# Performance work log

Hardware: AMD Instinct MI355X
Metric: run time of the kernel (lower is better)

## Reference

```python
import jax, jax.numpy as jnp
import numpy as np
from jax import lax

I, H, C = 1086, 16, 15


def _lstm_layer(x, w_ih, w_hh, b):
    # x: [B, T, in], w_ih: [4H, in], w_hh: [4H, H], b: [4H]  (b = b_ih + b_hh)
    B = x.shape[0]
    Hd = w_hh.shape[1]
    # precompute the big input projection outside the scan
    pre = jnp.einsum('bti,gi->btg', x, w_ih) + b  # [B, T, 4H]

    def step(carry, pt):
        h, c = carry
        gates = pt + h @ w_hh.T  # [B, 4H]
        i, f, g, o = jnp.split(gates, 4, axis=-1)  # torch gate order i,f,g,o
        i = jax.nn.sigmoid(i)
        f = jax.nn.sigmoid(f)
        g = jnp.tanh(g)
        o = jax.nn.sigmoid(o)
        c = f * c + i * g
        h = o * jnp.tanh(c)
        return (h, c), h

    h0 = jnp.zeros((B, Hd), x.dtype)
    c0 = jnp.zeros((B, Hd), x.dtype)
    _, ys = lax.scan(step, (h0, c0), jnp.swapaxes(pre, 0, 1))
    return jnp.swapaxes(ys, 0, 1)  # [B, T, H]


def setup_inputs() -> dict:
    key = jax.random.key(0)
    ks = jax.random.split(key, 20)
    s = 1.0 / np.sqrt(H)  # torch LSTM/Linear default init scale
    x = jax.random.normal(ks[0], (256, 200, I), dtype=jnp.float32)

    def w(k, shape):
        return jax.random.uniform(k, shape, jnp.float32, -s, s)

    inp = {'x': x}
    ins = [I, H, H, H]  # lstm1 layer0/1, lstm2 layer0/1
    names = ['l0a', 'l0b', 'l1a', 'l1b']
    ki = 1
    for n, d_in in zip(names, ins):
        inp['w_ih_' + n] = w(ks[ki], (4 * H, d_in)); ki += 1
        inp['w_hh_' + n] = w(ks[ki], (4 * H, H)); ki += 1
        inp['b_' + n] = w(ks[ki], (4 * H,)); ki += 1
    inp['w_fc1'] = w(ks[ki], (H, H)); ki += 1
    inp['b_fc1'] = w(ks[ki], (H,)); ki += 1
    inp['w_fc2'] = w(ks[ki], (C, H)); ki += 1
    inp['b_fc2'] = w(ks[ki], (C,))
    return inp


def reference(x, w_ih_l0a, w_hh_l0a, b_l0a, w_ih_l0b, w_hh_l0b, b_l0b,
              w_ih_l1a, w_hh_l1a, b_l1a, w_ih_l1b, w_hh_l1b, b_l1b,
              w_fc1, b_fc1, w_fc2, b_fc2):
    # lstm1 (2 layers), dropout between layers is identity in eval mode
    out = _lstm_layer(x, w_ih_l0a, w_hh_l0a, b_l0a)
    out = _lstm_layer(out, w_ih_l0b, w_hh_l0b, b_l0b)
    # lstm2 (2 layers)
    out = _lstm_layer(out, w_ih_l1a, w_hh_l1a, b_l1a)
    out = _lstm_layer(out, w_ih_l1b, w_hh_l1b, b_l1b)
    h_last = out[:, -1, :]  # [B, H]
    h = jax.nn.relu(h_last @ w_fc1.T + b_fc1)
    logits = h @ w_fc2.T + b_fc2  # [B, C]
    return jax.nn.softmax(logits, axis=1)
```

## Files before the change

### kernel.cpp

```cpp
#include <hip/hip_runtime.h>

#define T_STEPS 200
#define IN_DIM 1086

using f32x4v = __attribute__((ext_vector_type(4))) float;
using bf16x8 = __attribute__((ext_vector_type(8))) short;
using u32x4  = __attribute__((ext_vector_type(4))) unsigned int;
typedef unsigned uv2 __attribute__((ext_vector_type(2)));

#if __has_builtin(__builtin_amdgcn_permlane16_swap) && __has_builtin(__builtin_amdgcn_permlane32_swap)
#define HAVE_PERMLANE_SWAP 1
#else
#define HAVE_PERMLANE_SWAP 0
#endif

#if __has_builtin(__builtin_amdgcn_exp2f)
#define EXP2F(x) __builtin_amdgcn_exp2f(x)
#else
#define EXP2F(x) exp2f(x)
#endif

__device__ __forceinline__ float rl_f(float v, int lane) {
    return __uint_as_float((unsigned)__builtin_amdgcn_readlane((int)__float_as_uint(v), lane));
}

__global__ __launch_bounds__(256) void pre0_gemm(
    const float* __restrict__ X, const float* __restrict__ W,
    const float* __restrict__ bias, float* __restrict__ out)
{
    __shared__ unsigned short AhL[4][128][8];
    __shared__ unsigned short AlL[4][128][8];
    __shared__ unsigned short BhL[4][64][8];
    __shared__ unsigned short BlL[4][64][8];

    const int tid  = threadIdx.x;
    const int lane = tid & 63;
    const int wv   = tid >> 6;
    const long m0  = (long)blockIdx.x * 128;

    const int sr  = tid >> 1;
    const int skb = (tid & 1) * 16;
    const int wr  = sr & 63;
    const float* xsrc = X + (m0 + sr) * (long)IN_DIM + skb;
    const float* wsrc = W + (long)wr * IN_DIM + skb;

    const int fr = lane & 15;
    const int kg = lane >> 4;

    f32x4v acc[2][4];
    #pragma unroll
    for (int mf = 0; mf < 2; ++mf)
        #pragma unroll
        for (int nf = 0; nf < 4; ++nf)
            #pragma unroll
            for (int r = 0; r < 4; ++r) acc[mf][nf][r] = 0.0f;

    for (int k0 = 0; k0 < IN_DIM; k0 += 32) {
        float xv[16];
        #pragma unroll
        for (int j = 0; j < 16; j += 2) {
            int k = k0 + skb + j;
            if (k + 2 <= IN_DIM) {
                float2 t = *(const float2*)(xsrc + k0 + j);
                xv[j] = t.x; xv[j + 1] = t.y;
            } else { xv[j] = 0.0f; xv[j + 1] = 0.0f; }
        }
        float wvv[16];
        if (tid < 128) {
            #pragma unroll
            for (int j = 0; j < 16; j += 2) {
                int k = k0 + skb + j;
                if (k + 2 <= IN_DIM) {
                    float2 t = *(const float2*)(wsrc + k0 + j);
                    wvv[j] = t.x; wvv[j + 1] = t.y;
                } else { wvv[j] = 0.0f; wvv[j + 1] = 0.0f; }
            }
        }
        __syncthreads();

        #pragma unroll
        for (int q = 0; q < 2; ++q) {
            u32x4 hw, lw;
            #pragma unroll
            for (int p = 0; p < 4; ++p) {
                float a0 = xv[q * 8 + 2 * p], a1 = xv[q * 8 + 2 * p + 1];
                unsigned u0 = __float_as_uint(a0), u1 = __float_as_uint(a1);
                unsigned h0 = u0 & 0xffff0000u, h1 = u1 & 0xffff0000u;
                hw[p] = (u0 >> 16) | h1;
                float l0 = a0 - __uint_as_float(h0);
                float l1 = a1 - __uint_as_float(h1);
                lw[p] = (__float_as_uint(l0) >> 16) | (__float_as_uint(l1) & 0xffff0000u);
            }
            int kgs = (tid & 1) * 2 + q;
            *(u32x4*)&AhL[kgs][sr][0] = hw;
            *(u32x4*)&AlL[kgs][sr][0] = lw;
        }
        if (tid < 128) {
            #pragma unroll
            for (int q = 0; q < 2; ++q) {
                u32x4 hw, lw;
                #pragma unroll
                for (int p = 0; p < 4; ++p) {
                    float a0 = wvv[q * 8 + 2 * p], a1 = wvv[q * 8 + 2 * p + 1];
                    unsigned u0 = __float_as_uint(a0), u1 = __float_as_uint(a1);
                    unsigned h0 = u0 & 0xffff0000u, h1 = u1 & 0xffff0000u;
                    hw[p] = (u0 >> 16) | h1;
                    float l0 = a0 - __uint_as_float(h0);
                    float l1 = a1 - __uint_as_float(h1);
                    lw[p] = (__float_as_uint(l0) >> 16) | (__float_as_uint(l1) & 0xffff0000u);
                }
                int kgs = (tid & 1) * 2 + q;
                *(u32x4*)&BhL[kgs][wr][0] = hw;
                *(u32x4*)&BlL[kgs][wr][0] = lw;
            }
        }
        __syncthreads();

        bf16x8 ah[2], al[2], bh[4], bl[4];
        #pragma unroll
        for (int mf = 0; mf < 2; ++mf) {
            ah[mf] = *(const bf16x8*)&AhL[kg][wv * 32 + mf * 16 + fr][0];
            al[mf] = *(const bf16x8*)&AlL[kg][wv * 32 + mf * 16 + fr][0];
        }
        #pragma unroll
        for (int nf = 0; nf < 4; ++nf) {
            bh[nf] = *(const bf16x8*)&BhL[kg][nf * 16 + fr][0];
            bl[nf] = *(const bf16x8*)&BlL[kg][nf * 16 + fr][0];
        }
        #pragma unroll
        for (int mf = 0; mf < 2; ++mf)
            #pragma unroll
            for (int nf = 0; nf < 4; ++nf) {
                acc[mf][nf] = __builtin_amdgcn_mfma_f32_16x16x32_bf16(ah[mf], bh[nf], acc[mf][nf], 0, 0, 0);
                acc[mf][nf] = __builtin_amdgcn_mfma_f32_16x16x32_bf16(al[mf], bh[nf], acc[mf][nf], 0, 0, 0);
                acc[mf][nf] = __builtin_amdgcn_mfma_f32_16x16x32_bf16(ah[mf], bl[nf], acc[mf][nf], 0, 0, 0);
            }
    }

    float bvv[4];
    #pragma unroll
    for (int nf = 0; nf < 4; ++nf) bvv[nf] = bias[nf * 16 + fr];
    #pragma unroll
    for (int mf = 0; mf < 2; ++mf)
        #pragma unroll
        for (int nf = 0; nf < 4; ++nf)
            #pragma unroll
            for (int r = 0; r < 4; ++r) {
                long row = m0 + wv * 32 + mf * 16 + kg * 4 + r;
                out[row * 64 + nf * 16 + fr] = acc[mf][nf][r] + bvv[nf];
            }
}

__global__ __launch_bounds__(256) void mega_scan(
    const float* __restrict__ pre0, const float* __restrict__ whh0,
    const float* __restrict__ wih1, const float* __restrict__ whh1, const float* __restrict__ b1,
    const float* __restrict__ wih2, const float* __restrict__ whh2, const float* __restrict__ b2,
    const float* __restrict__ wih3, const float* __restrict__ whh3, const float* __restrict__ b3,
    const float* __restrict__ w_fc1, const float* __restrict__ b_fc1,
    const float* __restrict__ w_fc2, const float* __restrict__ b_fc2,
    float* __restrict__ out)
{
    __shared__ float buf[3][T_STEPS][16];

    const int b    = blockIdx.x;
    const int tid  = threadIdx.x;
    const int g    = tid & 63;
    const int wv   = tid >> 6;

    bool sel16 = false, sel32 = false;
#if HAVE_PERMLANE_SWAP
    {
        uv2 q16 = __builtin_amdgcn_permlane16_swap((unsigned)g, (unsigned)g, false, false);
        sel16 = (__builtin_amdgcn_readfirstlane((int)q16[1]) == 16);
        uv2 q32 = __builtin_amdgcn_permlane32_swap((unsigned)g, (unsigned)g, false, false);
        sel32 = (__builtin_amdgcn_readfirstlane((int)q32[1]) == 32);
    }
#endif

    const float* wih = nullptr; const float* whh; const float* bias = nullptr;
    if      (wv == 0) { whh = whh0; }
    else if (wv == 1) { wih = wih1; whh = whh1; bias = b1; }
    else if (wv == 2) { wih = wih2; whh = whh2; bias = b2; }
    else              { wih = wih3; whh = whh3; bias = b3; }

    float whh_r[16];
    #pragma unroll
    for (int q = 0; q < 4; ++q)
        *(float4*)&whh_r[q * 4] = *(const float4*)&whh[g * 16 + q * 4];
    float wih_r[16]; float bg = 0.0f;
    if (wv) {
        #pragma unroll
        for (int q = 0; q < 4; ++q)
            *(float4*)&wih_r[q * 4] = *(const float4*)&wih[g * 16 + q * 4];
        bg = bias[g];
    }

    const float* pb = pre0 + (long)b * T_STEPS * 64 + g;
    float pc = 0.0f, p1 = 0.0f, p2 = 0.0f;
    if (wv == 0) { pc = pb[0]; p1 = pb[64]; p2 = pb[128]; }

    float hs[16];
    #pragma unroll
    for (int k = 0; k < 16; ++k) hs[k] = 0.0f;
    float c = 0.0f;

    const int q4 = g >> 4;
    const float escale = (q4 == 2) ? -2.8853900817779268f : -1.4426950408889634f;
    const float am = (q4 == 2) ? 2.0f : 1.0f;
    const float aa = (q4 == 2) ? -1.0f : 0.0f;

    for (int tau = 0; tau < T_STEPS + 3; ++tau) {
        __syncthreads();
        const int t = tau - wv;
        if (t >= 0 && t < T_STEPS) {
            float xr[16];
            if (wv) {
                #pragma unroll
                for (int q = 0; q < 4; ++q)
                    *(float4*)&xr[q * 4] = *(const float4*)&buf[wv - 1][t][q * 4];
            }
            float r0 = fmaf(whh_r[0], hs[0], wv ? bg : pc);
            float r1 = whh_r[1] * hs[1];
            float r2 = whh_r[2] * hs[2];
            float r3 = whh_r[3] * hs[3];
            #pragma unroll
            for (int k = 4; k < 16; k += 4) {
                r0 = fmaf(whh_r[k + 0], hs[k + 0], r0);
                r1 = fmaf(whh_r[k + 1], hs[k + 1], r1);
                r2 = fmaf(whh_r[k + 2], hs[k + 2], r2);
                r3 = fmaf(whh_r[k + 3], hs[k + 3], r3);
            }
            float acc = (r0 + r1) + (r2 + r3);
            if (wv) {
                float p0 = wih_r[0] * xr[0];
                float q1 = wih_r[1] * xr[1];
                float q2 = wih_r[2] * xr[2];
                float q3 = wih_r[3] * xr[3];
                #pragma unroll
                for (int k = 4; k < 16; k += 4) {
                    p0 = fmaf(wih_r[k + 0], xr[k + 0], p0);
                    q1 = fmaf(wih_r[k + 1], xr[k + 1], q1);
                    q2 = fmaf(wih_r[k + 2], xr[k + 2], q2);
                    q3 = fmaf(wih_r[k + 3], xr[k + 3], q3);
                }
                acc += (p0 + q1) + (q2 + q3);
            }
            float e = EXP2F(escale * acc);
            float s = __builtin_amdgcn_rcpf(1.0f + e);
            float a = fmaf(am, s, aa);
#if HAVE_PERMLANE_SWAP
            unsigned au = __float_as_uint(a);
            uv2 r16 = __builtin_amdgcn_permlane16_swap(au, au, false, false);
            uv2 r32 = __builtin_amdgcn_permlane32_swap(au, au, false, false);
            unsigned fvu = sel16 ? r16[1] : r16[0];
            unsigned gvu = sel32 ? r32[1] : r32[0];
            uv2 r48 = __builtin_amdgcn_permlane16_swap(gvu, gvu, false, false);
            unsigned ovu = sel16 ? r48[1] : r48[0];
            float fv = __uint_as_float(fvu);
            float gv = __uint_as_float(gvu);
            float ov = __uint_as_float(ovu);
#else
            float fv = __shfl_xor(a, 16, 64);
            float gv = __shfl_xor(a, 32, 64);
            float ov = __shfl_xor(a, 48, 64);
#endif
            c = fmaf(fv, c, a * gv);
            float e2 = EXP2F(-2.8853900817779268f * c);
            float s2 = __builtin_amdgcn_rcpf(1.0f + e2);
            float hn = fmaf(ov + ov, s2, -ov);
            if (wv < 3 && g < 16) buf[wv][t][g] = hn;
            #pragma unroll
            for (int k = 0; k < 16; ++k) hs[k] = rl_f(hn, k);
            if (wv == 0) {
                pc = p1; p1 = p2;
                int tn = t + 3; tn = tn < T_STEPS ? tn : T_STEPS - 1;
                p2 = pb[(long)tn * 64];
            }
        }
    }

    if (wv == 3 && g < 16) {
        float a1 = b_fc1[g];
        #pragma unroll
        for (int k = 0; k < 16; ++k) a1 = fmaf(w_fc1[g * 16 + k], hs[k], a1);
        a1 = fmaxf(a1, 0.0f);
        float h1[16];
        #pragma unroll
        for (int k = 0; k < 16; ++k) h1[k] = rl_f(a1, k);
        float lg = -3.0e38f;
        if (g < 15) {
            lg = b_fc2[g];
            #pragma unroll
            for (int k = 0; k < 16; ++k) lg = fmaf(w_fc2[g * 16 + k], h1[k], lg);
        }
        float mx = lg;
        #pragma unroll
        for (int d = 8; d >= 1; d >>= 1) mx = fmaxf(mx, __shfl_xor(mx, d, 16));
        float ev = (g < 15) ? EXP2F(1.4426950408889634f * (lg - mx)) : 0.0f;
        float sm = ev;
        #pragma unroll
        for (int d = 8; d >= 1; d >>= 1) sm += __shfl_xor(sm, d, 16);
        if (g < 15) out[b * 15 + g] = ev * __builtin_amdgcn_rcpf(sm);
    }
}

extern "C" void kernel_launch(void* const* d_in, const int* in_sizes, int n_in,
                              void* d_out, int out_size, void* d_ws, size_t ws_size,
                              hipStream_t stream) {
    const float* x    = (const float*)d_in[0];
    const float* wih0 = (const float*)d_in[1];
    const float* whh0 = (const float*)d_in[2];
    const float* b0   = (const float*)d_in[3];
    const float* wih1 = (const float*)d_in[4];
    const float* whh1 = (const float*)d_in[5];
    const float* b1   = (const float*)d_in[6];
    const float* wih2 = (const float*)d_in[7];
    const float* whh2 = (const float*)d_in[8];
    const float* b2   = (const float*)d_in[9];
    const float* wih3 = (const float*)d_in[10];
    const float* whh3 = (const float*)d_in[11];
    const float* b3   = (const float*)d_in[12];
    const float* wfc1 = (const float*)d_in[13];
    const float* bfc1 = (const float*)d_in[14];
    const float* wfc2 = (const float*)d_in[15];
    const float* bfc2 = (const float*)d_in[16];

    float* pre0 = (float*)d_ws;

    pre0_gemm<<<dim3(400), dim3(256), 0, stream>>>(x, wih0, b0, pre0);
    mega_scan<<<dim3(256), dim3(256), 0, stream>>>(pre0, whh0,
        wih1, whh1, b1, wih2, whh2, b2, wih3, whh3, b3,
        wfc1, bfc1, wfc2, bfc2, (float*)d_out);
}
```

Baseline: 190.6 us.

## Prepack W_ih into bf16 hi/lo tiles and drop LDS staging in input GEMM

Adds a small prepack kernel that splits the layer-0 input weights into bf16 high/low halves in MFMA-ready tile order in the workspace. The input-projection GEMM becomes single-wave blocks of 32 rows that load X directly into registers, convert to hi/lo, and read prepacked weights from global memory. This removes LDS staging, both __syncthreads per k-tile, and the repeated per-block conversion of W. In exchange it adds a kernel launch and repeated global/L2 reads of the weights by each of 1600 blocks. The X loads are now strided per lane rather than cooperative.

```diff
diff --git a/kernel.cpp b/kernel.cpp
--- a/kernel.cpp
+++ b/kernel.cpp
@@ -2,6 +2,8 @@
 
 #define T_STEPS 200
 #define IN_DIM 1086
+#define KTILES 34
+#define M_TOTAL 51200
 
 using f32x4v = __attribute__((ext_vector_type(4))) float;
 using bf16x8 = __attribute__((ext_vector_type(8))) short;
@@ -24,28 +26,50 @@
     return __uint_as_float((unsigned)__builtin_amdgcn_readlane((int)__float_as_uint(v), lane));
 }
 
-__global__ __launch_bounds__(256) void pre0_gemm(
-    const float* __restrict__ X, const float* __restrict__ W,
+__global__ __launch_bounds__(256) void prepack_w(
+    const float* __restrict__ W,
+    unsigned short* __restrict__ Wh, unsigned short* __restrict__ Wl)
+{
+    int idx = blockIdx.x * 256 + threadIdx.x;
+    if (idx >= KTILES * 4 * 64 * 8) return;
+    int j = idx & 7;
+    int n = (idx >> 3) & 63;
+    int k = (idx >> 9) * 8 + j;
+    float v = (k < IN_DIM) ? W[n * IN_DIM + k] : 0.0f;
+    unsigned u = __float_as_uint(v);
+    unsigned hi = u & 0xffff0000u;
+    float lo = v - __uint_as_float(hi);
+    Wh[idx] = (unsigned short)(u >> 16);
+    Wl[idx] = (unsigned short)(__float_as_uint(lo) >> 16);
+}
+
+__device__ __forceinline__ void cvt_hilo(const float a[8], bf16x8& hv, bf16x8& lv) {
+    union { u32x4 u; bf16x8 v; } H, L;
+    #pragma unroll
+    for (int p = 0; p < 4; ++p) {
+        float a0 = a[2 * p], a1 = a[2 * p + 1];
+        unsigned u0 = __float_as_uint(a0), u1 = __float_as_uint(a1);
+        unsigned h0 = u0 & 0xffff0000u, h1 = u1 & 0xffff0000u;
+        H.u[p] = (u0 >> 16) | h1;
+        float l0 = a0 - __uint_as_float(h0);
+        float l1 = a1 - __uint_as_float(h1);
+        L.u[p] = (__float_as_uint(l0) >> 16) | (__float_as_uint(l1) & 0xffff0000u);
+    }
+    hv = H.v; lv = L.v;
+}
+
+__global__ __launch_bounds__(64) void pre0_gemm(
+    const float* __restrict__ X,
+    const unsigned short* __restrict__ Wh, const unsigned short* __restrict__ Wl,
     const float* __restrict__ bias, float* __restrict__ out)
 {
-    __shared__ unsigned short AhL[4][128][8];
-    __shared__ unsigned short AlL[4][128][8];
-    __shared__ unsigned short BhL[4][64][8];
-    __shared__ unsigned short BlL[4][64][8];
-
-    const int tid  = threadIdx.x;
-    const int lane = tid & 63;
-    const int wv   = tid >> 6;
-    const long m0  = (long)blockIdx.x * 128;
-
-    const int sr  = tid >> 1;
-    const int skb = (tid & 1) * 16;
-    const int wr  = sr & 63;
-    const float* xsrc = X + (m0 + sr) * (long)IN_DIM + skb;
-    const float* wsrc = W + (long)wr * IN_DIM + skb;
-
+    const int lane = threadIdx.x;
     const int fr = lane & 15;
     const int kg = lane >> 4;
+    const long m0 = (long)blockIdx.x * 32;
+
+    const float* xr0 = X + (m0 + fr) * (long)IN_DIM;
+    const float* xr1 = X + (m0 + 16 + fr) * (long)IN_DIM;
 
     f32x4v acc[2][4];
     #pragma unroll
@@ -55,86 +79,48 @@
             #pragma unroll
             for (int r = 0; r < 4; ++r) acc[mf][nf][r] = 0.0f;
 
-    for (int k0 = 0; k0 < IN_DIM; k0 += 32) {
-        float xv[16];
-        #pragma unroll
-        for (int j = 0; j < 16; j += 2) {
-            int k = k0 + skb + j;
-            if (k + 2 <= IN_DIM) {
-                float2 t = *(const float2*)(xsrc + k0 + j);
-                xv[j] = t.x; xv[j + 1] = t.y;
-            } else { xv[j] = 0.0f; xv[j + 1] = 0.0f; }
-        }
-        float wvv[16];
-        if (tid < 128) {
-            #pragma unroll
-            for (int j = 0; j < 16; j += 2) {
-                int k = k0 + skb + j;
-                if (k + 2 <= IN_DIM) {
-                    float2 t = *(const float2*)(wsrc + k0 + j);
-                    wvv[j] = t.x; wvv[j + 1] = t.y;
-                } else { wvv[j] = 0.0f; wvv[j + 1] = 0.0f; }
-            }
-        }
-        __syncthreads();
-
-        #pragma unroll
-        for (int q = 0; q < 2; ++q) {
-            u32x4 hw, lw;
-            #pragma unroll
-            for (int p = 0; p < 4; ++p) {
-                float a0 = xv[q * 8 + 2 * p], a1 = xv[q * 8 + 2 * p + 1];
-                unsigned u0 = __float_as_uint(a0), u1 = __float_as_uint(a1);
-                unsigned h0 = u0 & 0xffff0000u, h1 = u1 & 0xffff0000u;
-                hw[p] = (u0 >> 16) | h1;
-                float l0 = a0 - __uint_as_float(h0);
-                float l1 = a1 - __uint_as_float(h1);
-                lw[p] = (__float_as_uint(l0) >> 16) | (__float_as_uint(l1) & 0xffff0000u);
-            }
-            int kgs = (tid & 1) * 2 + q;
-            *(u32x4*)&AhL[kgs][sr][0] = hw;
-            *(u32x4*)&AlL[kgs][sr][0] = lw;
-        }
-        if (tid < 128) {
-            #pragma unroll
-            for (int q = 0; q < 2; ++q) {
-                u32x4 hw, lw;
-                #pragma unroll
-                for (int p = 0; p < 4; ++p) {
-                    float a0 = wvv[q * 8 + 2 * p], a1 = wvv[q * 8 + 2 * p + 1];
-                    unsigned u0 = __float_as_uint(a0), u1 = __float_as_uint(a1);
-                    unsigned h0 = u0 & 0xffff0000u, h1 = u1 & 0xffff0000u;
-                    hw[p] = (u0 >> 16) | h1;
-                    float l0 = a0 - __uint_as_float(h0);
-                    float l1 = a1 - __uint_as_float(h1);
-                    lw[p] = (__float_as_uint(l0) >> 16) | (__float_as_uint(l1) & 0xffff0000u);
-                }
-                int kgs = (tid & 1) * 2 + q;
-                *(u32x4*)&BhL[kgs][wr][0] = hw;
-                *(u32x4*)&BlL[kgs][wr][0] = lw;
-            }
-        }
-        __syncthreads();
-
-        bf16x8 ah[2], al[2], bh[4], bl[4];
-        #pragma unroll
-        for (int mf = 0; mf < 2; ++mf) {
-            ah[mf] = *(const bf16x8*)&AhL[kg][wv * 32 + mf * 16 + fr][0];
-            al[mf] = *(const bf16x8*)&AlL[kg][wv * 32 + mf * 16 + fr][0];
-        }
+    for (int kt = 0; kt < KTILES; ++kt) {
+        const int kb = kt * 32 + kg * 8;
+
+        float a0[8], a1[8];
+        if (kt < KTILES - 1) {
+            #pragma unroll
+            for (int q = 0; q < 4; ++q) {
+                float2 t0 = *(const float2*)(xr0 + kb + 2 * q);
+                float2 t1 = *(const float2*)(xr1 + kb + 2 * q);
+                a0[2 * q] = t0.x; a0[2 * q + 1] = t0.y;
+                a1[2 * q] = t1.x; a1[2 * q + 1] = t1.y;
+            }
+        } else {
+            #pragma unroll
+            for (int j = 0; j < 8; ++j) {
+                int k = kb + j;
+                a0[j] = (k < IN_DIM) ? xr0[k] : 0.0f;
+                a1[j] = (k < IN_DIM) ? xr1[k] : 0.0f;
+            }
+        }
+
+        const long bbase = (long)(kt * 4 + kg) * 64 * 8;
+        bf16x8 bh[4], bl[4];
         #pragma unroll
         for (int nf = 0; nf < 4; ++nf) {
-            bh[nf] = *(const bf16x8*)&BhL[kg][nf * 16 + fr][0];
-            bl[nf] = *(const bf16x8*)&BlL[kg][nf * 16 + fr][0];
-        }
-        #pragma unroll
-        for (int mf = 0; mf < 2; ++mf)
-            #pragma unroll
-            for (int nf = 0; nf < 4; ++nf) {
-                acc[mf][nf] = __builtin_amdgcn_mfma_f32_16x16x32_bf16(ah[mf], bh[nf], acc[mf][nf], 0, 0, 0);
-                acc[mf][nf] = __builtin_amdgcn_mfma_f32_16x16x32_bf16(al[mf], bh[nf], acc[mf][nf], 0, 0, 0);
-                acc[mf][nf] = __builtin_amdgcn_mfma_f32_16x16x32_bf16(ah[mf], bl[nf], acc[mf][nf], 0, 0, 0);
-            }
+            bh[nf] = *(const bf16x8*)(Wh + bbase + (nf * 16 + fr) * 8);
+            bl[nf] = *(const bf16x8*)(Wl + bbase + (nf * 16 + fr) * 8);
+        }
+
+        bf16x8 ah0, al0, ah1, al1;
+        cvt_hilo(a0, ah0, al0);
+        cvt_hilo(a1, ah1, al1);
+
+        #pragma unroll
+        for (int nf = 0; nf < 4; ++nf) {
+            acc[0][nf] = __builtin_amdgcn_mfma_f32_16x16x32_bf16(ah0, bh[nf], acc[0][nf], 0, 0, 0);
+            acc[0][nf] = __builtin_amdgcn_mfma_f32_16x16x32_bf16(al0, bh[nf], acc[0][nf], 0, 0, 0);
+            acc[0][nf] = __builtin_amdgcn_mfma_f32_16x16x32_bf16(ah0, bl[nf], acc[0][nf], 0, 0, 0);
+            acc[1][nf] = __builtin_amdgcn_mfma_f32_16x16x32_bf16(ah1, bh[nf], acc[1][nf], 0, 0, 0);
+            acc[1][nf] = __builtin_amdgcn_mfma_f32_16x16x32_bf16(al1, bh[nf], acc[1][nf], 0, 0, 0);
+            acc[1][nf] = __builtin_amdgcn_mfma_f32_16x16x32_bf16(ah1, bl[nf], acc[1][nf], 0, 0, 0);
+        }
     }
 
     float bvv[4];
@@ -146,7 +132,7 @@
         for (int nf = 0; nf < 4; ++nf)
             #pragma unroll
             for (int r = 0; r < 4; ++r) {
-                long row = m0 + wv * 32 + mf * 16 + kg * 4 + r;
+                long row = m0 + mf * 16 + kg * 4 + r;
                 out[row * 64 + nf * 16 + fr] = acc[mf][nf][r] + bvv[nf];
             }
 }
@@ -326,8 +312,11 @@
     const float* bfc2 = (const float*)d_in[16];
 
     float* pre0 = (float*)d_ws;
-
-    pre0_gemm<<<dim3(400), dim3(256), 0, stream>>>(x, wih0, b0, pre0);
+    unsigned short* Wh = (unsigned short*)((char*)d_ws + 13107200);
+    unsigned short* Wl = (unsigned short*)((char*)d_ws + 13107200 + 139264);
+
+    prepack_w<<<dim3((KTILES * 4 * 64 * 8 + 255) / 256), dim3(256), 0, stream>>>(wih0, Wh, Wl);
+    pre0_gemm<<<dim3(M_TOTAL / 32), dim3(64), 0, stream>>>(x, Wh, Wl, b0, pre0);
     mega_scan<<<dim3(256), dim3(256), 0, stream>>>(pre0, whh0,
         wih1, whh1, b1, wih2, whh2, b2, wih3, whh3, b3,
         wfc1, bfc1, wfc2, bfc2, (float*)d_out);
```

New measurement: 166.6 us. -12.6%, faster.
